# Kernel optimization log

Measured on AMD Instinct MI355X. Metric: run time of the kernel, lower is better.

## Reference

```python
import jax, jax.numpy as jnp
import numpy as np

N = 50000      # nodes
E = 800000     # edges (avg degree 16)
D = 64         # node feature dim
DE = 32        # edge feature dim
H = 256        # MLP hidden dim


def setup_inputs() -> dict:
    key = jax.random.key(0)
    k0, k1, k2, k3, k4 = jax.random.split(key, 5)
    x = jax.random.normal(k0, (N, D), dtype=jnp.float32)
    edge_index = jax.random.randint(k1, (2, E), 0, N)
    edge_attr = jax.random.normal(k2, (E, DE), dtype=jnp.float32)
    fan_in1 = 2 * D + DE  # 160
    W1 = jax.random.normal(k3, (fan_in1, H), dtype=jnp.float32) / np.float32(np.sqrt(fan_in1))
    b1 = jnp.zeros((H,), dtype=jnp.float32)
    W2 = jax.random.normal(k4, (H, D), dtype=jnp.float32) / np.float32(np.sqrt(H))
    b2 = jnp.zeros((D,), dtype=jnp.float32)
    return {"x": x, "edge_index": edge_index, "edge_attr": edge_attr,
            "W1": W1, "b1": b1, "W2": W2, "b2": b2}


def reference(x, edge_index, edge_attr, W1, b1, W2, b2):
    row, col = edge_index[0], edge_index[1]
    # gather endpoint features + edge features -> [E, 2D+DE]
    feats = jnp.concatenate([x[row], x[col], edge_attr], axis=-1)
    # MLP: Linear -> ReLU -> Linear
    h = jax.nn.relu(feats @ W1 + b1)          # [E, H]
    out = h @ W2 + b2                          # [E, D]
    # scatter-max aggregate by source node (row), dim_size = N
    agg = jax.ops.segment_max(out, row, num_segments=N)  # [N, D]
    # PyG's old scatter_('max') zero-fills empty slots
    agg = jnp.where(jnp.isneginf(agg), jnp.float32(0.0), agg)
    return (agg, out)
```

## Files before the change

kernel.cpp:

```cpp
#include <hip/hip_runtime.h>
#include <math.h>

#define NNODES 50000
#define NEDGES 800000

using short8 = __attribute__((ext_vector_type(8))) short;
using f32x4  = __attribute__((ext_vector_type(4))) float;

__device__ __forceinline__ short f2b(float v) {
    unsigned u = __builtin_bit_cast(unsigned, v);
    u = (u + 0x7FFFu + ((u >> 16) & 1u)) >> 16;
    return (short)u;
}

__device__ __forceinline__ unsigned pk2(short a, short b) {
    return (unsigned)(unsigned short)a | ((unsigned)(unsigned short)b << 16);
}

__global__ void prep_x(const float* __restrict__ x, short* __restrict__ xb) {
    int i = blockIdx.x * 256 + threadIdx.x;
    if (i < NNODES * 64 / 4) {
        float4 v = reinterpret_cast<const float4*>(x)[i];
        short4 o;
        o.x = f2b(v.x); o.y = f2b(v.y); o.z = f2b(v.z); o.w = f2b(v.w);
        reinterpret_cast<short4*>(xb)[i] = o;
    }
}

__global__ void prep_w(const float* __restrict__ W1, const float* __restrict__ W2,
                       short* __restrict__ wpk) {
    int i = blockIdx.x * 256 + threadIdx.x;
    if (i < 40960) {
        int k = i >> 8, n = i & 255;
        wpk[((n >> 4) * 20 + (k >> 3)) * 128 + (n & 15) * 8 + (k & 7)] = f2b(W1[i]);
    }
    if (i < 16384) {
        int k = i >> 6, n = i & 63;
        wpk[40960 + ((n >> 4) * 32 + (k >> 3)) * 128 + (n & 15) * 8 + (k & 7)] = f2b(W2[i]);
    }
}

__global__ void csr_count(const int* __restrict__ ei, unsigned* __restrict__ cnt) {
    int e = blockIdx.x * 256 + threadIdx.x;
    if (e < NEDGES) atomicAdd(&cnt[ei[e]], 1u);
}

__global__ __launch_bounds__(1024)
void csr_scan1(const unsigned* __restrict__ cnt, unsigned* __restrict__ offs,
               unsigned* __restrict__ bsum) {
    __shared__ unsigned sbuf[1024];
    int t = threadIdx.x, i = blockIdx.x * 1024 + t;
    unsigned v = (i < NNODES) ? cnt[i] : 0u;
    sbuf[t] = v;
    __syncthreads();
    for (int off = 1; off < 1024; off <<= 1) {
        unsigned add = (t >= off) ? sbuf[t - off] : 0u;
        __syncthreads();
        sbuf[t] += add;
        __syncthreads();
    }
    if (i < NNODES) offs[i] = sbuf[t];
    if (t == 1023) bsum[blockIdx.x] = sbuf[1023];
}

__global__ void csr_scan2(unsigned* __restrict__ bsum) {
    int t = threadIdx.x;
    unsigned v = (t < 49) ? bsum[t] : 0u;
    unsigned orig = v;
    for (int off = 1; off < 64; off <<= 1) {
        unsigned n = __shfl_up(v, off, 64);
        if (t >= off) v += n;
    }
    if (t < 49) bsum[t] = v - orig;
}

__global__ __launch_bounds__(1024)
void csr_scan3(const unsigned* __restrict__ cnt, unsigned* __restrict__ offs,
               const unsigned* __restrict__ bsum) {
    int i = blockIdx.x * 1024 + threadIdx.x;
    if (i < NNODES)       offs[i] = offs[i] - cnt[i] + bsum[blockIdx.x];
    else if (i == NNODES) offs[i] = NEDGES;
}

__global__ void csr_place(const int* __restrict__ ei, const unsigned* __restrict__ offs,
                          unsigned* __restrict__ cur, unsigned* __restrict__ elist) {
    int e = blockIdx.x * 256 + threadIdx.x;
    if (e < NEDGES) {
        int r = ei[e];
        unsigned p = offs[r] + atomicAdd(&cur[r], 1u);
        elist[p] = (unsigned)e;
    }
}

__global__ __launch_bounds__(256, 4)
void edgeconv_main(const short* __restrict__ xb, const int* __restrict__ ei,
                   const float* __restrict__ ea, const short* __restrict__ wpk,
                   const float* __restrict__ b1, const float* __restrict__ b2,
                   float* __restrict__ outbuf)
{
    __shared__ char hbuf[4][32 * 80];

    const int tid  = threadIdx.x;
    const int wave = tid >> 6, lane = tid & 63;
    const int l16 = lane & 15, lg = lane >> 4;
    char* hw = hbuf[wave];
    const short* w2a = wpk + 40960;

    const int ebase = (blockIdx.x * 4 + wave) * 32;

    short8 fx[2][5];
    #pragma unroll
    for (int nf = 0; nf < 2; ++nf) {
        int e = ebase + nf * 16 + l16;
        int r = ei[e], cc = ei[NEDGES + e];
        fx[nf][0] = *reinterpret_cast<const short8*>(xb + r * 64 + lg * 8);
        fx[nf][1] = *reinterpret_cast<const short8*>(xb + r * 64 + 32 + lg * 8);
        fx[nf][2] = *reinterpret_cast<const short8*>(xb + cc * 64 + lg * 8);
        fx[nf][3] = *reinterpret_cast<const short8*>(xb + cc * 64 + 32 + lg * 8);
        const float4* eap = reinterpret_cast<const float4*>(ea + e * 32 + lg * 8);
        float4 va = eap[0], vb = eap[1];
        short8 f;
        f[0]=f2b(va.x); f[1]=f2b(va.y); f[2]=f2b(va.z); f[3]=f2b(va.w);
        f[4]=f2b(vb.x); f[5]=f2b(vb.y); f[6]=f2b(vb.z); f[7]=f2b(vb.w);
        fx[nf][4] = f;
    }

    f32x4 acc2[4][2] = {};

    #pragma unroll 1
    for (int hp = 0; hp < 8; ++hp) {
        f32x4 acc1[2][2] = {};
        #pragma unroll
        for (int kk = 0; kk < 5; ++kk) {
            #pragma unroll
            for (int mt = 0; mt < 2; ++mt) {
                int nt = hp * 2 + mt;
                short8 wf = *reinterpret_cast<const short8*>(
                    wpk + (nt * 20 + kk * 4 + lg) * 128 + l16 * 8);
                acc1[mt][0] = __builtin_amdgcn_mfma_f32_16x16x32_bf16(wf, fx[0][kk], acc1[mt][0], 0, 0, 0);
                acc1[mt][1] = __builtin_amdgcn_mfma_f32_16x16x32_bf16(wf, fx[1][kk], acc1[mt][1], 0, 0, 0);
            }
        }
        #pragma unroll
        for (int mt = 0; mt < 2; ++mt) {
            float4 bb = *reinterpret_cast<const float4*>(b1 + hp * 32 + mt * 16 + lg * 4);
            #pragma unroll
            for (int nf = 0; nf < 2; ++nf) {
                float v0 = fmaxf(acc1[mt][nf][0] + bb.x, 0.0f);
                float v1 = fmaxf(acc1[mt][nf][1] + bb.y, 0.0f);
                float v2 = fmaxf(acc1[mt][nf][2] + bb.z, 0.0f);
                float v3 = fmaxf(acc1[mt][nf][3] + bb.w, 0.0f);
                unsigned long long p =
                    (unsigned long long)pk2(f2b(v0), f2b(v1)) |
                    ((unsigned long long)pk2(f2b(v2), f2b(v3)) << 32);
                *reinterpret_cast<unsigned long long*>(
                    hw + (nf * 16 + l16) * 80 + mt * 32 + lg * 8) = p;
            }
        }
        asm volatile("s_waitcnt lgkmcnt(0)" ::: "memory");

        short8 hfr0 = *reinterpret_cast<const short8*>(hw + l16 * 80 + lg * 16);
        short8 hfr1 = *reinterpret_cast<const short8*>(hw + (16 + l16) * 80 + lg * 16);
        #pragma unroll
        for (int mt2 = 0; mt2 < 4; ++mt2) {
            short8 wf2 = *reinterpret_cast<const short8*>(
                w2a + (mt2 * 32 + hp * 4 + lg) * 128 + l16 * 8);
            acc2[mt2][0] = __builtin_amdgcn_mfma_f32_16x16x32_bf16(wf2, hfr0, acc2[mt2][0], 0, 0, 0);
            acc2[mt2][1] = __builtin_amdgcn_mfma_f32_16x16x32_bf16(wf2, hfr1, acc2[mt2][1], 0, 0, 0);
        }
        asm volatile("" ::: "memory");
    }

    #pragma unroll
    for (int mt2 = 0; mt2 < 4; ++mt2) {
        float4 bb = *reinterpret_cast<const float4*>(b2 + mt2 * 16 + lg * 4);
        #pragma unroll
        for (int nf = 0; nf < 2; ++nf) {
            int e = ebase + nf * 16 + l16;
            f32x4 v;
            v[0] = acc2[mt2][nf][0] + bb.x;
            v[1] = acc2[mt2][nf][1] + bb.y;
            v[2] = acc2[mt2][nf][2] + bb.z;
            v[3] = acc2[mt2][nf][3] + bb.w;
            __builtin_nontemporal_store(v,
                reinterpret_cast<f32x4*>(outbuf + e * 64 + mt2 * 16 + lg * 4));
        }
    }
}

__global__ __launch_bounds__(256)
void agg_max(const unsigned* __restrict__ offs, const unsigned* __restrict__ elist,
             const float* __restrict__ outbuf, float* __restrict__ agg)
{
    const int wave = threadIdx.x >> 6, lane = threadIdx.x & 63;
    const int node = blockIdx.x * 4 + wave;
    if (node >= NNODES) return;
    const unsigned s = offs[node], eend = offs[node + 1];
    float m = -INFINITY;
    for (unsigned p = s; p < eend; ++p) {
        unsigned e = elist[p];
        m = fmaxf(m, outbuf[(size_t)e * 64 + lane]);
    }
    agg[(size_t)node * 64 + lane] = (s == eend) ? 0.0f : m;
}

extern "C" void kernel_launch(void* const* d_in, const int* in_sizes, int n_in,
                              void* d_out, int out_size, void* d_ws, size_t ws_size,
                              hipStream_t stream)
{
    const float* x  = (const float*)d_in[0];
    const int*   ei = (const int*)d_in[1];
    const float* ea = (const float*)d_in[2];
    const float* W1 = (const float*)d_in[3];
    const float* b1 = (const float*)d_in[4];
    const float* W2 = (const float*)d_in[5];
    const float* b2 = (const float*)d_in[6];

    float* aggp = (float*)d_out;
    float* outp = aggp + (size_t)NNODES * 64;

    short*    xb   = (short*)d_ws;
    short*    wpk  = (short*)((char*)d_ws + 6400000);
    unsigned* meta = (unsigned*)((char*)d_ws + 6514688);
    unsigned* cnt   = meta;
    unsigned* cur   = meta + 50000;
    unsigned* offs  = meta + 100000;
    unsigned* bsum  = meta + 150016;
    unsigned* elist = meta + 150144;

    hipMemsetAsync(cnt, 0, 100000 * sizeof(unsigned), stream);
    prep_x<<<NNODES * 64 / 4 / 256, 256, 0, stream>>>(x, xb);
    prep_w<<<160, 256, 0, stream>>>(W1, W2, wpk);
    csr_count<<<NEDGES / 256, 256, 0, stream>>>(ei, cnt);
    csr_scan1<<<49, 1024, 0, stream>>>(cnt, offs, bsum);
    csr_scan2<<<1, 64, 0, stream>>>(bsum);
    csr_scan3<<<49, 1024, 0, stream>>>(cnt, offs, bsum);
    csr_place<<<NEDGES / 256, 256, 0, stream>>>(ei, offs, cur, elist);
    edgeconv_main<<<NEDGES / 128, 256, 0, stream>>>(xb, ei, ea, wpk, b1, b2, outp);
    agg_max<<<(NNODES + 3) / 4, 256, 0, stream>>>(offs, elist, outp, aggp);
}
```

Before: 352.4 us.

## Stage MLP weights in LDS with persistent 1024-thread blocks; fold biases into accumulators

```diff
diff --git a/kernel.cpp b/kernel.cpp
--- a/kernel.cpp
+++ b/kernel.cpp
@@ -1,16 +1,17 @@
 #include <hip/hip_runtime.h>
+#include <hip/hip_bf16.h>
 #include <math.h>
 
 #define NNODES 50000
 #define NEDGES 800000
+#define CHUNKS (NEDGES / 32)
+#define GWAVES 4096
 
 using short8 = __attribute__((ext_vector_type(8))) short;
 using f32x4  = __attribute__((ext_vector_type(4))) float;
 
 __device__ __forceinline__ short f2b(float v) {
-    unsigned u = __builtin_bit_cast(unsigned, v);
-    u = (u + 0x7FFFu + ((u >> 16) & 1u)) >> 16;
-    return (short)u;
+    return __builtin_bit_cast(short, __float2bfloat16(v));
 }
 
 __device__ __forceinline__ unsigned pk2(short a, short b) {
@@ -92,98 +93,112 @@
     }
 }
 
-__global__ __launch_bounds__(256, 4)
+__global__ __launch_bounds__(1024, 4)
 void edgeconv_main(const short* __restrict__ xb, const int* __restrict__ ei,
                    const float* __restrict__ ea, const short* __restrict__ wpk,
                    const float* __restrict__ b1, const float* __restrict__ b2,
                    float* __restrict__ outbuf)
 {
-    __shared__ char hbuf[4][32 * 80];
-
-    const int tid  = threadIdx.x;
+    __shared__ short wlds[57344];
+    __shared__ char  hbuf[16][2560];
+
+    const int tid = threadIdx.x;
+    for (int i = tid; i < 7168; i += 1024)
+        reinterpret_cast<short8*>(wlds)[i] = reinterpret_cast<const short8*>(wpk)[i];
+    __syncthreads();
+
+    const short* w1s = wlds;
+    const short* w2s = wlds + 40960;
     const int wave = tid >> 6, lane = tid & 63;
     const int l16 = lane & 15, lg = lane >> 4;
     char* hw = hbuf[wave];
-    const short* w2a = wpk + 40960;
-
-    const int ebase = (blockIdx.x * 4 + wave) * 32;
-
-    short8 fx[2][5];
-    #pragma unroll
-    for (int nf = 0; nf < 2; ++nf) {
-        int e = ebase + nf * 16 + l16;
-        int r = ei[e], cc = ei[NEDGES + e];
-        fx[nf][0] = *reinterpret_cast<const short8*>(xb + r * 64 + lg * 8);
-        fx[nf][1] = *reinterpret_cast<const short8*>(xb + r * 64 + 32 + lg * 8);
-        fx[nf][2] = *reinterpret_cast<const short8*>(xb + cc * 64 + lg * 8);
-        fx[nf][3] = *reinterpret_cast<const short8*>(xb + cc * 64 + 32 + lg * 8);
-        const float4* eap = reinterpret_cast<const float4*>(ea + e * 32 + lg * 8);
-        float4 va = eap[0], vb = eap[1];
-        short8 f;
-        f[0]=f2b(va.x); f[1]=f2b(va.y); f[2]=f2b(va.z); f[3]=f2b(va.w);
-        f[4]=f2b(vb.x); f[5]=f2b(vb.y); f[6]=f2b(vb.z); f[7]=f2b(vb.w);
-        fx[nf][4] = f;
-    }
-
-    f32x4 acc2[4][2] = {};
-
-    #pragma unroll 1
-    for (int hp = 0; hp < 8; ++hp) {
-        f32x4 acc1[2][2] = {};
-        #pragma unroll
-        for (int kk = 0; kk < 5; ++kk) {
-            #pragma unroll
-            for (int mt = 0; mt < 2; ++mt) {
-                int nt = hp * 2 + mt;
-                short8 wf = *reinterpret_cast<const short8*>(
-                    wpk + (nt * 20 + kk * 4 + lg) * 128 + l16 * 8);
-                acc1[mt][0] = __builtin_amdgcn_mfma_f32_16x16x32_bf16(wf, fx[0][kk], acc1[mt][0], 0, 0, 0);
-                acc1[mt][1] = __builtin_amdgcn_mfma_f32_16x16x32_bf16(wf, fx[1][kk], acc1[mt][1], 0, 0, 0);
-            }
-        }
-        #pragma unroll
-        for (int mt = 0; mt < 2; ++mt) {
-            float4 bb = *reinterpret_cast<const float4*>(b1 + hp * 32 + mt * 16 + lg * 4);
-            #pragma unroll
-            for (int nf = 0; nf < 2; ++nf) {
-                float v0 = fmaxf(acc1[mt][nf][0] + bb.x, 0.0f);
-                float v1 = fmaxf(acc1[mt][nf][1] + bb.y, 0.0f);
-                float v2 = fmaxf(acc1[mt][nf][2] + bb.z, 0.0f);
-                float v3 = fmaxf(acc1[mt][nf][3] + bb.w, 0.0f);
-                unsigned long long p =
-                    (unsigned long long)pk2(f2b(v0), f2b(v1)) |
-                    ((unsigned long long)pk2(f2b(v2), f2b(v3)) << 32);
-                *reinterpret_cast<unsigned long long*>(
-                    hw + (nf * 16 + l16) * 80 + mt * 32 + lg * 8) = p;
-            }
-        }
-        asm volatile("s_waitcnt lgkmcnt(0)" ::: "memory");
-
-        short8 hfr0 = *reinterpret_cast<const short8*>(hw + l16 * 80 + lg * 16);
-        short8 hfr1 = *reinterpret_cast<const short8*>(hw + (16 + l16) * 80 + lg * 16);
-        #pragma unroll
-        for (int mt2 = 0; mt2 < 4; ++mt2) {
-            short8 wf2 = *reinterpret_cast<const short8*>(
-                w2a + (mt2 * 32 + hp * 4 + lg) * 128 + l16 * 8);
-            acc2[mt2][0] = __builtin_amdgcn_mfma_f32_16x16x32_bf16(wf2, hfr0, acc2[mt2][0], 0, 0, 0);
-            acc2[mt2][1] = __builtin_amdgcn_mfma_f32_16x16x32_bf16(wf2, hfr1, acc2[mt2][1], 0, 0, 0);
-        }
-        asm volatile("" ::: "memory");
-    }
-
-    #pragma unroll
-    for (int mt2 = 0; mt2 < 4; ++mt2) {
-        float4 bb = *reinterpret_cast<const float4*>(b2 + mt2 * 16 + lg * 4);
+    const int gw = blockIdx.x * 16 + wave;
+
+    for (int c = gw; c < CHUNKS; c += GWAVES) {
+        const int ebase = c * 32;
+
+        short8 fx[2][5];
         #pragma unroll
         for (int nf = 0; nf < 2; ++nf) {
             int e = ebase + nf * 16 + l16;
-            f32x4 v;
-            v[0] = acc2[mt2][nf][0] + bb.x;
-            v[1] = acc2[mt2][nf][1] + bb.y;
-            v[2] = acc2[mt2][nf][2] + bb.z;
-            v[3] = acc2[mt2][nf][3] + bb.w;
-            __builtin_nontemporal_store(v,
-                reinterpret_cast<f32x4*>(outbuf + e * 64 + mt2 * 16 + lg * 4));
+            int r = ei[e], cc = ei[NEDGES + e];
+            fx[nf][0] = *reinterpret_cast<const short8*>(xb + r * 64 + lg * 8);
+            fx[nf][1] = *reinterpret_cast<const short8*>(xb + r * 64 + 32 + lg * 8);
+            fx[nf][2] = *reinterpret_cast<const short8*>(xb + cc * 64 + lg * 8);
+            fx[nf][3] = *reinterpret_cast<const short8*>(xb + cc * 64 + 32 + lg * 8);
+            const float4* eap = reinterpret_cast<const float4*>(ea + e * 32 + lg * 8);
+            float4 va = eap[0], vb = eap[1];
+            short8 f;
+            f[0]=f2b(va.x); f[1]=f2b(va.y); f[2]=f2b(va.z); f[3]=f2b(va.w);
+            f[4]=f2b(vb.x); f[5]=f2b(vb.y); f[6]=f2b(vb.z); f[7]=f2b(vb.w);
+            fx[nf][4] = f;
+        }
+
+        f32x4 acc2[4][2];
+        #pragma unroll
+        for (int mt2 = 0; mt2 < 4; ++mt2) {
+            float4 bb = *reinterpret_cast<const float4*>(b2 + mt2 * 16 + lg * 4);
+            f32x4 bi; bi[0] = bb.x; bi[1] = bb.y; bi[2] = bb.z; bi[3] = bb.w;
+            acc2[mt2][0] = bi; acc2[mt2][1] = bi;
+        }
+
+        #pragma unroll 1
+        for (int hp = 0; hp < 8; ++hp) {
+            f32x4 acc1[2][2];
+            #pragma unroll
+            for (int mt = 0; mt < 2; ++mt) {
+                float4 bb = *reinterpret_cast<const float4*>(b1 + hp * 32 + mt * 16 + lg * 4);
+                f32x4 bi; bi[0] = bb.x; bi[1] = bb.y; bi[2] = bb.z; bi[3] = bb.w;
+                acc1[mt][0] = bi; acc1[mt][1] = bi;
+            }
+            #pragma unroll
+            for (int kk = 0; kk < 5; ++kk) {
+                #pragma unroll
+                for (int mt = 0; mt < 2; ++mt) {
+                    int nt = hp * 2 + mt;
+                    short8 wf = *reinterpret_cast<const short8*>(
+                        w1s + (nt * 20 + kk * 4 + lg) * 128 + l16 * 8);
+                    acc1[mt][0] = __builtin_amdgcn_mfma_f32_16x16x32_bf16(wf, fx[0][kk], acc1[mt][0], 0, 0, 0);
+                    acc1[mt][1] = __builtin_amdgcn_mfma_f32_16x16x32_bf16(wf, fx[1][kk], acc1[mt][1], 0, 0, 0);
+                }
+            }
+            #pragma unroll
+            for (int mt = 0; mt < 2; ++mt) {
+                #pragma unroll
+                for (int nf = 0; nf < 2; ++nf) {
+                    float v0 = fmaxf(acc1[mt][nf][0], 0.0f);
+                    float v1 = fmaxf(acc1[mt][nf][1], 0.0f);
+                    float v2 = fmaxf(acc1[mt][nf][2], 0.0f);
+                    float v3 = fmaxf(acc1[mt][nf][3], 0.0f);
+                    unsigned long long p =
+                        (unsigned long long)pk2(f2b(v0), f2b(v1)) |
+                        ((unsigned long long)pk2(f2b(v2), f2b(v3)) << 32);
+                    *reinterpret_cast<unsigned long long*>(
+                        hw + (nf * 16 + l16) * 80 + mt * 32 + lg * 8) = p;
+                }
+            }
+            asm volatile("s_waitcnt lgkmcnt(0)" ::: "memory");
+
+            short8 hfr0 = *reinterpret_cast<const short8*>(hw + l16 * 80 + lg * 16);
+            short8 hfr1 = *reinterpret_cast<const short8*>(hw + (16 + l16) * 80 + lg * 16);
+            #pragma unroll
+            for (int mt2 = 0; mt2 < 4; ++mt2) {
+                short8 wf2 = *reinterpret_cast<const short8*>(
+                    w2s + (mt2 * 32 + hp * 4 + lg) * 128 + l16 * 8);
+                acc2[mt2][0] = __builtin_amdgcn_mfma_f32_16x16x32_bf16(wf2, hfr0, acc2[mt2][0], 0, 0, 0);
+                acc2[mt2][1] = __builtin_amdgcn_mfma_f32_16x16x32_bf16(wf2, hfr1, acc2[mt2][1], 0, 0, 0);
+            }
+            asm volatile("" ::: "memory");
+        }
+
+        #pragma unroll
+        for (int mt2 = 0; mt2 < 4; ++mt2) {
+            #pragma unroll
+            for (int nf = 0; nf < 2; ++nf) {
+                int e = ebase + nf * 16 + l16;
+                __builtin_nontemporal_store(acc2[mt2][nf],
+                    reinterpret_cast<f32x4*>(outbuf + e * 64 + mt2 * 16 + lg * 4));
+            }
         }
     }
 }
@@ -196,11 +211,17 @@
     const int node = blockIdx.x * 4 + wave;
     if (node >= NNODES) return;
     const unsigned s = offs[node], eend = offs[node + 1];
-    float m = -INFINITY;
-    for (unsigned p = s; p < eend; ++p) {
-        unsigned e = elist[p];
-        m = fmaxf(m, outbuf[(size_t)e * 64 + lane]);
-    }
+    float m0 = -INFINITY, m1 = -INFINITY;
+    unsigned p = s;
+    for (; p + 2 <= eend; p += 2) {
+        unsigned e0 = elist[p], e1 = elist[p + 1];
+        float a = outbuf[(size_t)e0 * 64 + lane];
+        float b = outbuf[(size_t)e1 * 64 + lane];
+        m0 = fmaxf(m0, a);
+        m1 = fmaxf(m1, b);
+    }
+    if (p < eend) m0 = fmaxf(m0, outbuf[(size_t)elist[p] * 64 + lane]);
+    float m = fmaxf(m0, m1);
     agg[(size_t)node * 64 + lane] = (s == eend) ? 0.0f : m;
 }
 
@@ -236,6 +257,6 @@
     csr_scan2<<<1, 64, 0, stream>>>(bsum);
     csr_scan3<<<49, 1024, 0, stream>>>(cnt, offs, bsum);
     csr_place<<<NEDGES / 256, 256, 0, stream>>>(ei, offs, cur, elist);
-    edgeconv_main<<<NEDGES / 128, 256, 0, stream>>>(xb, ei, ea, wpk, b1, b2, outp);
+    edgeconv_main<<<256, 1024, 0, stream>>>(xb, ei, ea, wpk, b1, b2, outp);
     agg_max<<<(NNODES + 3) / 4, 256, 0, stream>>>(offs, elist, outp, aggp);
 }
```

New measurement: 327.2 us. 7.1% less time.
